# Kernel optimization log

Measured on AMD Instinct MI355X. Metric: run time of the kernel, lower is better.

Reference implementation:

```python
import jax, jax.numpy as jnp
import numpy as np

B, S, D, H, E, K = 8, 2048, 512, 2048, 8, 2


def setup_inputs() -> dict:
    key = jax.random.key(0)
    ks = jax.random.split(key, 6)
    x = jax.random.normal(ks[0], (B, S, D), dtype=jnp.float32)
    # HashRouter output: top-k expert assignments per token (int ids in [0, E))
    assign = jax.random.randint(ks[1], (B, S, K), 0, E, dtype=jnp.int64)
    # Stacked per-expert MLP params: Linear(D,H) -> ReLU -> Linear(H,D)
    s1 = 1.0 / np.sqrt(D)
    s2 = 1.0 / np.sqrt(H)
    W1 = jax.random.uniform(ks[2], (E, D, H), jnp.float32, -s1, s1)
    b1 = jax.random.uniform(ks[3], (E, H), jnp.float32, -s1, s1)
    W2 = jax.random.uniform(ks[4], (E, H, D), jnp.float32, -s2, s2)
    b2 = jax.random.uniform(ks[5], (E, D), jnp.float32, -s2, s2)
    return {"x": x, "assign": assign, "W1": W1, "b1": b1, "W2": W2, "b2": b2}


def reference(x, assign, W1, b1, W2, b2):
    b, s, d = x.shape
    e_total = W1.shape[0]
    k = assign.shape[-1]
    xf = x.reshape(b * s, d)                 # [N, D]
    af = assign.reshape(b * s, k)            # [N, K]
    out = jnp.zeros_like(xf)
    # Loop over fixed, small number of experts (structurally distinct params).
    for e in range(e_total):
        mask = (af == e).any(-1)             # token selected by expert e (once, even if both slots)
        h = jax.nn.relu(xf @ W1[e] + b1[e])  # [N, H]
        y = h @ W2[e] + b2[e]                # [N, D]
        out = out + jnp.where(mask[:, None], y, jnp.zeros((), y.dtype))
    return (out / k).reshape(b, s, d)
```

## Files before the change

### kernel.cpp

```cpp
#include <hip/hip_runtime.h>
#include <hip/hip_bf16.h>
#include <stdint.h>

#define E_NUM 8
#define D_DIM 512
#define H_DIM 2048
#define NTOK 16384

typedef __bf16 bf16;
typedef __bf16 bf16x8 __attribute__((ext_vector_type(8)));
typedef float  f32x4  __attribute__((ext_vector_type(4)));

#define BM 256
#define BN 256
#define BK 64

typedef __attribute__((address_space(1))) const void* gas_cp;
typedef __attribute__((address_space(3))) void* las_p;
__device__ __forceinline__ void gl_lds16(const void* g, void* l) {
  __builtin_amdgcn_global_load_lds((gas_cp)g, (las_p)l, 16, 0, 0);
}

static const size_t OFF_FILL = 32;
static const size_t OFF_LIST = 128;
static const size_t OFF_XBF  = 1ull << 20;
static const size_t OFF_W1T  = OFF_XBF + (size_t)NTOK*D_DIM*2;
static const size_t OFF_W2T  = OFF_W1T + (size_t)E_NUM*H_DIM*D_DIM*2;
static const size_t OFF_HBUF = OFF_W2T + (size_t)E_NUM*H_DIM*D_DIM*2;

__device__ __forceinline__ int rowbase_of(const int* cnt, int e) {
  int acc = 0;
  for (int i = 0; i < e; i++) acc += (cnt[i] + BM - 1) & ~(BM - 1);
  return acc;
}

__global__ void fill_kernel(const int* __restrict__ assign, int* __restrict__ fill,
                            int* __restrict__ lists) {
  int n = blockIdx.x * blockDim.x + threadIdx.x;
  int lane = threadIdx.x & 63;
  unsigned long long below = ((unsigned long long)1 << lane) - 1;
  int e0 = assign[2*n], e1 = assign[2*n+1];
  #pragma unroll
  for (int e = 0; e < E_NUM; e++) {
    bool h0 = (e0 == e);
    bool h1 = (e1 == e) && (e1 != e0);
    unsigned long long m0 = __ballot(h0);
    unsigned long long m1 = __ballot(h1);
    int c = __popcll(m0) + __popcll(m1);
    if (c > 0) {
      int leader = __ffsll((long long)(m0 | m1)) - 1;
      int b = 0;
      if (lane == leader) b = atomicAdd(&fill[e], c);
      b = __shfl(b, leader);
      if (h0) lists[e * NTOK + b + __popcll(m0 & below)] = n;
      if (h1) lists[e * NTOK + b + __popcll(m0) + __popcll(m1 & below)] = n;
    }
  }
}

__global__ void cvt_x(const float* __restrict__ x, bf16* __restrict__ xbf) {
  size_t i = ((size_t)blockIdx.x * 256 + threadIdx.x) * 8;
  float4 a = *reinterpret_cast<const float4*>(x + i);
  float4 b = *reinterpret_cast<const float4*>(x + i + 4);
  bf16x8 o;
  o[0] = (bf16)a.x; o[1] = (bf16)a.y; o[2] = (bf16)a.z; o[3] = (bf16)a.w;
  o[4] = (bf16)b.x; o[5] = (bf16)b.y; o[6] = (bf16)b.z; o[7] = (bf16)b.w;
  *reinterpret_cast<bf16x8*>(xbf + i) = o;
}

__global__ void transpose_cvt(const float* __restrict__ in, bf16* __restrict__ out,
                              int R, int C) {
  __shared__ float tile[32][33];
  int e = blockIdx.z;
  int c0 = blockIdx.x * 32, r0 = blockIdx.y * 32;
  const float* src = in + (size_t)e * R * C;
  bf16* dst = out + (size_t)e * R * C;
  int tx = threadIdx.x, ty = threadIdx.y;
  #pragma unroll
  for (int i = 0; i < 32; i += 8)
    tile[ty + i][tx] = src[(size_t)(r0 + ty + i) * C + c0 + tx];
  __syncthreads();
  #pragma unroll
  for (int i = 0; i < 32; i += 8)
    dst[(size_t)(c0 + ty + i) * R + r0 + tx] = (bf16)tile[tx][ty + i];
}

#define NC1 (H_DIM / BN)
__global__ __launch_bounds__(512, 2) void gemm1(
    const bf16* __restrict__ xbf, const bf16* __restrict__ w1t,
    const float* __restrict__ b1, const int* __restrict__ lists,
    const int* __restrict__ cnt, bf16* __restrict__ hbuf) {
  int lin = blockIdx.x;
  int xcd = lin & 7;
  int rem = lin >> 3;
  int nc  = rem & (NC1 - 1);
  int rb  = (rem >> 3) * 8 + xcd;
  int e   = rb >> 6;
  int m0  = (rb & 63) * BM;
  int ce  = cnt[e];
  if (m0 >= ce) return;
  int n0 = nc * BN;
  int rbase = rowbase_of(cnt, e);

  __shared__ bf16 xs[2][BM * BK];
  __shared__ bf16 bs[2][BN * BK];
  __shared__ int tok[BM];

  int tid = threadIdx.x;
  if (tid < BM) {
    int r = m0 + tid;
    tok[tid] = (r < ce) ? lists[e * NTOK + r] : lists[e * NTOK];
  }
  __syncthreads();

  const bf16* w1e = w1t + (size_t)e * H_DIM * D_DIM + (size_t)n0 * D_DIM;
  int wave = tid >> 6, lane = tid & 63;
  int quad = lane >> 4, l16 = lane & 15;
  int lr = lane >> 3;
  int lcs = (((lane & 7) ^ lr)) * 8;
  int wm = (wave >> 2) * 128, wn = (wave & 3) * 64;
  int l7 = l16 & 7;
  f32x4 acc[8][4] = {};

  auto stage = [&](int buf, int k0) {
    #pragma unroll
    for (int i = 0; i < 4; i++) {
      int s = wave * 4 + i;
      int t = tok[s * 8 + lr];
      gl_lds16(xbf + (size_t)t * D_DIM + k0 + lcs, &xs[buf][s * 512]);
    }
    #pragma unroll
    for (int i = 0; i < 4; i++) {
      int s = wave * 4 + i;
      gl_lds16(w1e + (size_t)(s * 8 + lr) * D_DIM + k0 + lcs, &bs[buf][s * 512]);
    }
  };

  const int nk = D_DIM / BK;
  stage(0, 0);
  for (int ki = 0; ki < nk; ki++) {
    __syncthreads();
    if (ki + 1 < nk) stage((ki + 1) & 1, (ki + 1) * BK);
    const bf16* xsc = xs[ki & 1];
    const bf16* bsc = bs[ki & 1];
    #pragma unroll
    for (int kk = 0; kk < BK; kk += 32) {
      int sw = ((quad + (kk >> 3)) ^ l7) * 8;
      bf16x8 bfr[4];
      #pragma unroll
      for (int j = 0; j < 4; j++)
        bfr[j] = *reinterpret_cast<const bf16x8*>(&bsc[(wn + j * 16 + l16) * BK + sw]);
      #pragma unroll
      for (int i = 0; i < 8; i++) {
        bf16x8 af = *reinterpret_cast<const bf16x8*>(&xsc[(wm + i * 16 + l16) * BK + sw]);
        #pragma unroll
        for (int j = 0; j < 4; j++)
          acc[i][j] = __builtin_amdgcn_mfma_f32_16x16x32_bf16(af, bfr[j], acc[i][j], 0, 0, 0);
      }
    }
  }

  bf16* hrow = hbuf + (size_t)(rbase + m0) * H_DIM;
  #pragma unroll
  for (int i = 0; i < 8; i++) {
    int row = wm + i * 16 + quad * 4;
    #pragma unroll
    for (int j = 0; j < 4; j++) {
      int col = n0 + wn + j * 16 + l16;
      float bias = b1[e * H_DIM + col];
      #pragma unroll
      for (int r = 0; r < 4; r++) {
        float v = acc[i][j][r] + bias;
        v = v > 0.f ? v : 0.f;
        hrow[(size_t)(row + r) * H_DIM + col] = (bf16)v;
      }
    }
  }
}

#define NC2 (D_DIM / BN)
__global__ __launch_bounds__(512, 2) void gemm2(
    const bf16* __restrict__ hbuf, const bf16* __restrict__ w2t,
    const float* __restrict__ b2, const int* __restrict__ lists,
    const int* __restrict__ cnt, float* __restrict__ out) {
  int lin = blockIdx.x;
  int xcd = lin & 7;
  int rem = lin >> 3;
  int nc  = rem & (NC2 - 1);
  int rb  = (rem >> 1) * 8 + xcd;
  int e   = rb >> 6;
  int m0  = (rb & 63) * BM;
  int ce  = cnt[e];
  if (m0 >= ce) return;
  int n0 = nc * BN;
  int rbase = rowbase_of(cnt, e);

  __shared__ bf16 hs[2][BM * BK];
  __shared__ bf16 bs[2][BN * BK];
  __shared__ int tok[BM];

  int tid = threadIdx.x;
  if (tid < BM) {
    int r = m0 + tid;
    tok[tid] = (r < ce) ? lists[e * NTOK + r] : -1;
  }
  __syncthreads();

  const bf16* hbase = hbuf + (size_t)(rbase + m0) * H_DIM;
  const bf16* w2e = w2t + (size_t)e * H_DIM * D_DIM + (size_t)n0 * H_DIM;
  int wave = tid >> 6, lane = tid & 63;
  int quad = lane >> 4, l16 = lane & 15;
  int lr = lane >> 3;
  int lcs = (((lane & 7) ^ lr)) * 8;
  int wm = (wave >> 2) * 128, wn = (wave & 3) * 64;
  int l7 = l16 & 7;
  f32x4 acc[8][4] = {};

  auto stage = [&](int buf, int k0) {
    #pragma unroll
    for (int i = 0; i < 4; i++) {
      int s = wave * 4 + i;
      gl_lds16(hbase + (size_t)(s * 8 + lr) * H_DIM + k0 + lcs, &hs[buf][s * 512]);
    }
    #pragma unroll
    for (int i = 0; i < 4; i++) {
      int s = wave * 4 + i;
      gl_lds16(w2e + (size_t)(s * 8 + lr) * H_DIM + k0 + lcs, &bs[buf][s * 512]);
    }
  };

  const int nk = H_DIM / BK;
  stage(0, 0);
  for (int ki = 0; ki < nk; ki++) {
    __syncthreads();
    if (ki + 1 < nk) stage((ki + 1) & 1, (ki + 1) * BK);
    const bf16* hsc = hs[ki & 1];
    const bf16* bsc = bs[ki & 1];
    #pragma unroll
    for (int kk = 0; kk < BK; kk += 32) {
      int sw = ((quad + (kk >> 3)) ^ l7) * 8;
      bf16x8 bfr[4];
      #pragma unroll
      for (int j = 0; j < 4; j++)
        bfr[j] = *reinterpret_cast<const bf16x8*>(&bsc[(wn + j * 16 + l16) * BK + sw]);
      #pragma unroll
      for (int i = 0; i < 8; i++) {
        bf16x8 af = *reinterpret_cast<const bf16x8*>(&hsc[(wm + i * 16 + l16) * BK + sw]);
        #pragma unroll
        for (int j = 0; j < 4; j++)
          acc[i][j] = __builtin_amdgcn_mfma_f32_16x16x32_bf16(af, bfr[j], acc[i][j], 0, 0, 0);
      }
    }
  }

  #pragma unroll
  for (int i = 0; i < 8; i++) {
    int row = wm + i * 16 + quad * 4;
    #pragma unroll
    for (int j = 0; j < 4; j++) {
      int col = n0 + wn + j * 16 + l16;
      float bias = b2[e * D_DIM + col];
      #pragma unroll
      for (int r = 0; r < 4; r++) {
        int t = tok[row + r];
        if (t >= 0) {
          float v = 0.5f * (acc[i][j][r] + bias);
          atomicAdd(&out[(size_t)t * D_DIM + col], v);
        }
      }
    }
  }
}

extern "C" void kernel_launch(void* const* d_in, const int* in_sizes, int n_in,
                              void* d_out, int out_size, void* d_ws, size_t ws_size,
                              hipStream_t stream) {
  const float* x      = (const float*)d_in[0];
  const int*   assign = (const int*)d_in[1];
  const float* W1     = (const float*)d_in[2];
  const float* b1     = (const float*)d_in[3];
  const float* W2     = (const float*)d_in[4];
  const float* b2     = (const float*)d_in[5];
  float* out = (float*)d_out;
  char* ws = (char*)d_ws;

  int* fill    = (int*)(ws + OFF_FILL);
  int* lists   = (int*)(ws + OFF_LIST);
  bf16* xbf    = (bf16*)(ws + OFF_XBF);
  bf16* w1t    = (bf16*)(ws + OFF_W1T);
  bf16* w2t    = (bf16*)(ws + OFF_W2T);
  bf16* hbuf   = (bf16*)(ws + OFF_HBUF);

  hipMemsetAsync(ws, 0, 128, stream);
  hipMemsetAsync(d_out, 0, (size_t)out_size * sizeof(float), stream);

  fill_kernel<<<NTOK / 256, 256, 0, stream>>>(assign, fill, lists);

  cvt_x<<<(NTOK * D_DIM) / (256 * 8), 256, 0, stream>>>(x, xbf);
  transpose_cvt<<<dim3(H_DIM / 32, D_DIM / 32, E_NUM), dim3(32, 8), 0, stream>>>(W1, w1t, D_DIM, H_DIM);
  transpose_cvt<<<dim3(D_DIM / 32, H_DIM / 32, E_NUM), dim3(32, 8), 0, stream>>>(W2, w2t, H_DIM, D_DIM);

  gemm1<<<(E_NUM * NTOK / BM) * NC1, 512, 0, stream>>>(xbf, w1t, b1, lists, fill, hbuf);
  gemm2<<<(E_NUM * NTOK / BM) * NC2, 512, 0, stream>>>(hbuf, w2t, b2, lists, fill, out);

  (void)in_sizes; (void)n_in; (void)ws_size;
}
```

Before: 399.2 us.

## Deepen GEMM pipeline with two-stage prefetch, explicit waitcnt and register-staged fragments

Both expert GEMM kernels now keep two tiles in flight: a new tile is issued two iterations ahead and a partial vmcnt wait replaces the full __syncthreads drain. All LDS fragments for the tile are read into registers first, then a barrier frees the buffer so the next global-to-LDS load can start while the MFMAs run, with setprio raising wave priority during the math. Per-row source pointers are precomputed outside the loop to cut address arithmetic. In exchange, register pressure rises from holding 24 bf16x8 fragments, and correctness relies on the hand-written vmcnt counts matching the 8 loads issued per stage.

New measurement: 450.1 us. 1.13x slower.

```diff
diff --git a/kernel.cpp b/kernel.cpp
--- a/kernel.cpp
+++ b/kernel.cpp
@@ -120,44 +120,59 @@
   int lcs = (((lane & 7) ^ lr)) * 8;
   int wm = (wave >> 2) * 128, wn = (wave & 3) * 64;
   int l7 = l16 & 7;
+
+  const bf16* asrc[4]; const bf16* bsrc[4]; int soff[4];
+  #pragma unroll
+  for (int i = 0; i < 4; i++) {
+    int s = wave * 4 + i;
+    asrc[i] = xbf + (size_t)tok[s * 8 + lr] * D_DIM + lcs;
+    bsrc[i] = w1e + (size_t)(s * 8 + lr) * D_DIM + lcs;
+    soff[i] = s * 512;
+  }
+  auto stage = [&](int buf, int k0) {
+    #pragma unroll
+    for (int i = 0; i < 4; i++) gl_lds16(asrc[i] + k0, &xs[buf][soff[i]]);
+    #pragma unroll
+    for (int i = 0; i < 4; i++) gl_lds16(bsrc[i] + k0, &bs[buf][soff[i]]);
+  };
+
   f32x4 acc[8][4] = {};
-
-  auto stage = [&](int buf, int k0) {
-    #pragma unroll
-    for (int i = 0; i < 4; i++) {
-      int s = wave * 4 + i;
-      int t = tok[s * 8 + lr];
-      gl_lds16(xbf + (size_t)t * D_DIM + k0 + lcs, &xs[buf][s * 512]);
-    }
-    #pragma unroll
-    for (int i = 0; i < 4; i++) {
-      int s = wave * 4 + i;
-      gl_lds16(w1e + (size_t)(s * 8 + lr) * D_DIM + k0 + lcs, &bs[buf][s * 512]);
-    }
-  };
-
   const int nk = D_DIM / BK;
   stage(0, 0);
-  for (int ki = 0; ki < nk; ki++) {
-    __syncthreads();
-    if (ki + 1 < nk) stage((ki + 1) & 1, (ki + 1) * BK);
-    const bf16* xsc = xs[ki & 1];
-    const bf16* bsc = bs[ki & 1];
-    #pragma unroll
-    for (int kk = 0; kk < BK; kk += 32) {
-      int sw = ((quad + (kk >> 3)) ^ l7) * 8;
-      bf16x8 bfr[4];
+  stage(1, BK);
+  for (int t = 0; t < nk; t++) {
+    if (t + 1 < nk) { asm volatile("s_waitcnt vmcnt(8)" ::: "memory"); }
+    else            { asm volatile("s_waitcnt vmcnt(0)" ::: "memory"); }
+    __builtin_amdgcn_sched_barrier(0);
+    __builtin_amdgcn_s_barrier();
+    __builtin_amdgcn_sched_barrier(0);
+    const bf16* xsc = xs[t & 1];
+    const bf16* bsc = bs[t & 1];
+    bf16x8 af[2][8], bfr[2][4];
+    #pragma unroll
+    for (int k2 = 0; k2 < 2; k2++) {
+      int sw = ((quad + k2 * 4) ^ l7) * 8;
       #pragma unroll
       for (int j = 0; j < 4; j++)
-        bfr[j] = *reinterpret_cast<const bf16x8*>(&bsc[(wn + j * 16 + l16) * BK + sw]);
-      #pragma unroll
-      for (int i = 0; i < 8; i++) {
-        bf16x8 af = *reinterpret_cast<const bf16x8*>(&xsc[(wm + i * 16 + l16) * BK + sw]);
+        bfr[k2][j] = *reinterpret_cast<const bf16x8*>(&bsc[(wn + j * 16 + l16) * BK + sw]);
+      #pragma unroll
+      for (int i = 0; i < 8; i++)
+        af[k2][i] = *reinterpret_cast<const bf16x8*>(&xsc[(wm + i * 16 + l16) * BK + sw]);
+    }
+    asm volatile("s_waitcnt lgkmcnt(0)" ::: "memory");
+    __builtin_amdgcn_sched_barrier(0);
+    __builtin_amdgcn_s_barrier();
+    __builtin_amdgcn_sched_barrier(0);
+    if (t + 2 < nk) stage(t & 1, (t + 2) * BK);
+    __builtin_amdgcn_s_setprio(1);
+    #pragma unroll
+    for (int k2 = 0; k2 < 2; k2++)
+      #pragma unroll
+      for (int i = 0; i < 8; i++)
         #pragma unroll
         for (int j = 0; j < 4; j++)
-          acc[i][j] = __builtin_amdgcn_mfma_f32_16x16x32_bf16(af, bfr[j], acc[i][j], 0, 0, 0);
-      }
-    }
+          acc[i][j] = __builtin_amdgcn_mfma_f32_16x16x32_bf16(af[k2][i], bfr[k2][j], acc[i][j], 0, 0, 0);
+    __builtin_amdgcn_s_setprio(0);
   }
 
   bf16* hrow = hbuf + (size_t)(rbase + m0) * H_DIM;
@@ -214,43 +229,59 @@
   int lcs = (((lane & 7) ^ lr)) * 8;
   int wm = (wave >> 2) * 128, wn = (wave & 3) * 64;
   int l7 = l16 & 7;
+
+  const bf16* asrc[4]; const bf16* bsrc[4]; int soff[4];
+  #pragma unroll
+  for (int i = 0; i < 4; i++) {
+    int s = wave * 4 + i;
+    asrc[i] = hbase + (size_t)(s * 8 + lr) * H_DIM + lcs;
+    bsrc[i] = w2e + (size_t)(s * 8 + lr) * H_DIM + lcs;
+    soff[i] = s * 512;
+  }
+  auto stage = [&](int buf, int k0) {
+    #pragma unroll
+    for (int i = 0; i < 4; i++) gl_lds16(asrc[i] + k0, &hs[buf][soff[i]]);
+    #pragma unroll
+    for (int i = 0; i < 4; i++) gl_lds16(bsrc[i] + k0, &bs[buf][soff[i]]);
+  };
+
   f32x4 acc[8][4] = {};
-
-  auto stage = [&](int buf, int k0) {
-    #pragma unroll
-    for (int i = 0; i < 4; i++) {
-      int s = wave * 4 + i;
-      gl_lds16(hbase + (size_t)(s * 8 + lr) * H_DIM + k0 + lcs, &hs[buf][s * 512]);
-    }
-    #pragma unroll
-    for (int i = 0; i < 4; i++) {
-      int s = wave * 4 + i;
-      gl_lds16(w2e + (size_t)(s * 8 + lr) * H_DIM + k0 + lcs, &bs[buf][s * 512]);
-    }
-  };
-
   const int nk = H_DIM / BK;
   stage(0, 0);
-  for (int ki = 0; ki < nk; ki++) {
-    __syncthreads();
-    if (ki + 1 < nk) stage((ki + 1) & 1, (ki + 1) * BK);
-    const bf16* hsc = hs[ki & 1];
-    const bf16* bsc = bs[ki & 1];
-    #pragma unroll
-    for (int kk = 0; kk < BK; kk += 32) {
-      int sw = ((quad + (kk >> 3)) ^ l7) * 8;
-      bf16x8 bfr[4];
+  stage(1, BK);
+  for (int t = 0; t < nk; t++) {
+    if (t + 1 < nk) { asm volatile("s_waitcnt vmcnt(8)" ::: "memory"); }
+    else            { asm volatile("s_waitcnt vmcnt(0)" ::: "memory"); }
+    __builtin_amdgcn_sched_barrier(0);
+    __builtin_amdgcn_s_barrier();
+    __builtin_amdgcn_sched_barrier(0);
+    const bf16* hsc = hs[t & 1];
+    const bf16* bsc = bs[t & 1];
+    bf16x8 af[2][8], bfr[2][4];
+    #pragma unroll
+    for (int k2 = 0; k2 < 2; k2++) {
+      int sw = ((quad + k2 * 4) ^ l7) * 8;
       #pragma unroll
       for (int j = 0; j < 4; j++)
-        bfr[j] = *reinterpret_cast<const bf16x8*>(&bsc[(wn + j * 16 + l16) * BK + sw]);
-      #pragma unroll
-      for (int i = 0; i < 8; i++) {
-        bf16x8 af = *reinterpret_cast<const bf16x8*>(&hsc[(wm + i * 16 + l16) * BK + sw]);
+        bfr[k2][j] = *reinterpret_cast<const bf16x8*>(&bsc[(wn + j * 16 + l16) * BK + sw]);
+      #pragma unroll
+      for (int i = 0; i < 8; i++)
+        af[k2][i] = *reinterpret_cast<const bf16x8*>(&hsc[(wm + i * 16 + l16) * BK + sw]);
+    }
+    asm volatile("s_waitcnt lgkmcnt(0)" ::: "memory");
+    __builtin_amdgcn_sched_barrier(0);
+    __builtin_amdgcn_s_barrier();
+    __builtin_amdgcn_sched_barrier(0);
+    if (t + 2 < nk) stage(t & 1, (t + 2) * BK);
+    __builtin_amdgcn_s_setprio(1);
+    #pragma unroll
+    for (int k2 = 0; k2 < 2; k2++)
+      #pragma unroll
+      for (int i = 0; i < 8; i++)
         #pragma unroll
         for (int j = 0; j < 4; j++)
-          acc[i][j] = __builtin_amdgcn_mfma_f32_16x16x32_bf16(af, bfr[j], acc[i][j], 0, 0, 0);
-      }
-    }
+          acc[i][j] = __builtin_amdgcn_mfma_f32_16x16x32_bf16(af[k2][i], bfr[k2][j], acc[i][j], 0, 0, 0);
+    __builtin_amdgcn_s_setprio(0);
   }
 
   #pragma unroll
```
